# Kernel tuning notes

Measured on AMD Instinct MI355X. Metric: run time of the kernel, lower is better.

Reference implementation:

```python
import jax, jax.numpy as jnp
import numpy as np

N_NODES = 50000
N_EDGES = 800000
NEG_SLOPE = 0.2


def _gat_layer(x, src, dst, W, al, ar, n_nodes):
    """Single multi-head GAT conv (DGL-style). Returns [N, H, D]."""
    H, D = al.shape
    feat = (x @ W).reshape(n_nodes, H, D)              # [N,H,D]
    el = jnp.einsum('nhd,hd->nh', feat, al)            # [N,H]
    er = jnp.einsum('nhd,hd->nh', feat, ar)            # [N,H]
    e = jax.nn.leaky_relu(el[src] + er[dst], NEG_SLOPE)  # [E,H]
    # numerically-stable edge softmax over incoming edges per dst node
    emax = jax.ops.segment_max(e, dst, num_segments=n_nodes)  # [N,H]
    emax = jnp.where(jnp.isfinite(emax), emax, 0.0)
    ee = jnp.exp(e - emax[dst])                        # [E,H]
    denom = jax.ops.segment_sum(ee, dst, num_segments=n_nodes)  # [N,H]
    alpha = ee / (denom[dst] + 1e-9)                   # [E,H]
    msg = alpha[:, :, None] * feat[src]                # [E,H,D]
    return jax.ops.segment_sum(msg, dst, num_segments=n_nodes)  # [N,H,D]


def setup_inputs() -> dict:
    key = jax.random.key(0)
    ks = jax.random.split(key, 9)
    features = jax.random.normal(ks[0], (N_NODES, 512), jnp.float32)
    src = jax.random.randint(ks[1], (N_EDGES,), 0, N_NODES)
    dst = jax.random.randint(ks[2], (N_EDGES,), 0, N_NODES)
    W1 = jax.random.normal(ks[3], (512, 256), jnp.float32) * 0.05
    al1 = jax.random.normal(ks[4], (8, 32), jnp.float32) * 0.05
    ar1 = jax.random.normal(ks[5], (8, 32), jnp.float32) * 0.05
    W2 = jax.random.normal(ks[6], (256, 320), jnp.float32) * 0.05
    al2 = jax.random.normal(ks[7], (8, 40), jnp.float32) * 0.05
    ar2 = jax.random.normal(ks[8], (8, 40), jnp.float32) * 0.05
    return {"features": features, "src": src, "dst": dst,
            "W1": W1, "al1": al1, "ar1": ar1,
            "W2": W2, "al2": al2, "ar2": ar2}


def reference(features, src, dst, W1, al1, ar1, W2, al2, ar2):
    n = features.shape[0]
    h = _gat_layer(features, src, dst, W1, al1, ar1, n)   # [N,8,32]
    h = jax.nn.elu(h.reshape(n, -1))                      # flatten(1) + ELU -> [N,256]
    h = _gat_layer(h, src, dst, W2, al2, ar2, n)          # [N,8,40]
    return h.mean(axis=1)                                 # head mean -> [N,40]
```

## Files before the change

kernel.cpp:

```cpp
#include <hip/hip_runtime.h>
#include <math.h>

typedef float f32x4 __attribute__((ext_vector_type(4)));
typedef __bf16 bf16x2 __attribute__((ext_vector_type(2)));
typedef __bf16 bf16x4 __attribute__((ext_vector_type(4)));
typedef __bf16 bf16x8 __attribute__((ext_vector_type(8)));


__global__ void hist_kernel(const int* __restrict__ dst, int* __restrict__ cnt, int E) {
    int e = blockIdx.x * blockDim.x + threadIdx.x;
    if (e < E) atomicAdd(&cnt[dst[e]], 1);
}

__global__ __launch_bounds__(256) void scan_blk(const int* __restrict__ cnt,
                                                int* __restrict__ incl,
                                                int* __restrict__ bsum, int n) {
    __shared__ int sd[256];
    const int t = threadIdx.x;
    int i = blockIdx.x * 256 + t;
    int v = (i < n) ? cnt[i] : 0;
    sd[t] = v;
    __syncthreads();
#pragma unroll
    for (int off = 1; off < 256; off <<= 1) {
        int x = (t >= off) ? sd[t - off] : 0;
        __syncthreads();
        sd[t] += x;
        __syncthreads();
    }
    if (i < n) incl[i] = sd[t];
    if (t == 255) bsum[blockIdx.x] = sd[255];
}

__global__ __launch_bounds__(256) void scan_top(const int* __restrict__ bsum,
                                                int* __restrict__ boff, int nb) {
    __shared__ int sd[256];
    const int t = threadIdx.x;
    int v = (t < nb) ? bsum[t] : 0;
    sd[t] = v;
    __syncthreads();
#pragma unroll
    for (int off = 1; off < 256; off <<= 1) {
        int x = (t >= off) ? sd[t - off] : 0;
        __syncthreads();
        sd[t] += x;
        __syncthreads();
    }
    if (t < nb) boff[t] = sd[t] - v;
}

__global__ void scan_fix(const int* __restrict__ incl, const int* __restrict__ boff,
                         const int* __restrict__ cnt, int* __restrict__ row_ptr,
                         int* __restrict__ cursor, int n) {
    int i = blockIdx.x * blockDim.x + threadIdx.x;
    if (i >= n) return;
    int total = incl[i] + boff[i >> 8];
    row_ptr[i + 1] = total;
    cursor[i] = total - cnt[i];
    if (i == 0) row_ptr[0] = 0;
}

__global__ void fill_kernel(const int* __restrict__ src, const int* __restrict__ dst,
                            int* __restrict__ cursor, int* __restrict__ ssrc, int E) {
    int e = blockIdx.x * blockDim.x + threadIdx.x;
    if (e < E) {
        int pos = atomicAdd(&cursor[dst[e]], 1);
        ssrc[pos] = src[e];
    }
}

__global__ void pack_b_kernel(const float* __restrict__ W, __bf16* __restrict__ Bh,
                              int K, int N) {
    int idx = blockIdx.x * blockDim.x + threadIdx.x;
    if (idx >= K * N) return;
    int e = idx & 7;
    int l = (idx >> 3) & 63;
    int c = idx >> 9;
    int ng = N >> 4;
    int g = c % ng;
    int k0 = (c / ng) << 5;
    int col = g * 16 + (l & 15);
    int k = k0 + ((l >> 4) << 3) + e;
    Bh[idx] = (__bf16)W[(size_t)k * N + col];
}

__device__ __forceinline__ int swz6(int x) { return x ^ (x >> 3); }

template <int BN, int NREP, bool FP32A>
__global__ __launch_bounds__(256, 4) void gemm_fused(
    const float* __restrict__ Af, const __bf16* __restrict__ Ahg,
    const __bf16* __restrict__ Alg, const __bf16* __restrict__ Bph,
    const float* __restrict__ al, const float* __restrict__ ar,
    __bf16* __restrict__ featb, float* __restrict__ el, float* __restrict__ er,
    int M, int K) {
    constexpr int WN = NREP * 16;
    constexpr int D = BN / 8;

    struct StageT {
        __bf16 Ah[2][2][64][8];
        __bf16 Al[2][2][64][8];
    };
    union Smem {
        StageT s;
        float ctile[4][16][WN + 1];
    };
    __shared__ __align__(16) Smem u;

    const int t = threadIdx.x;
    const int lane = t & 63;
    const int wid = t >> 6;
    const int row0 = blockIdx.x * 32;
    const int colw = wid * WN;
    const int fr = lane & 15;
    const int kq = lane >> 4;
    const int sr = t >> 3;
    const int kc = (t & 7) * 4;
    const int m_s = sr >> 4;
    const int xs = (sr & 15) + 16 * (kc >> 3);
    const int e0 = kc & 7;

    float4 av;
    bf16x4 avh, avl;

    auto loadA = [&](int k0) {
        int gr = row0 + sr;
        if (gr >= M) gr = M - 1;
        if constexpr (FP32A) {
            av = *(const float4*)&Af[(size_t)gr * K + k0 + kc];
        } else {
            avh = *(const bf16x4*)&Ahg[(size_t)gr * K + k0 + kc];
            avl = *(const bf16x4*)&Alg[(size_t)gr * K + k0 + kc];
        }
    };
    auto storeA = [&](int p) {
        if constexpr (FP32A) {
            __bf16 h0 = (__bf16)av.x, h1 = (__bf16)av.y, h2 = (__bf16)av.z,
                   h3 = (__bf16)av.w;
            bf16x4 hv = {h0, h1, h2, h3};
            bf16x4 lv = {(__bf16)(av.x - (float)h0), (__bf16)(av.y - (float)h1),
                         (__bf16)(av.z - (float)h2), (__bf16)(av.w - (float)h3)};
            *(bf16x4*)&u.s.Ah[p][m_s][swz6(xs)][e0] = hv;
            *(bf16x4*)&u.s.Al[p][m_s][swz6(xs)][e0] = lv;
        } else {
            *(bf16x4*)&u.s.Ah[p][m_s][swz6(xs)][e0] = avh;
            *(bf16x4*)&u.s.Al[p][m_s][swz6(xs)][e0] = avl;
        }
    };

    f32x4 acc[2][NREP] = {};

    loadA(0);
    int p = 0;
    for (int k0 = 0; k0 < K; k0 += 32) {
        bf16x8 bh[NREP];
        const int c0 = (k0 >> 5) * (BN >> 4) + wid * NREP;
#pragma unroll
        for (int n = 0; n < NREP; ++n)
            bh[n] = *(const bf16x8*)&Bph[(size_t)(c0 + n) * 512 + lane * 8];
        storeA(p);
        if (k0 + 32 < K) loadA(k0 + 32);
        __syncthreads();
        const int sl_ = swz6(lane);
        bf16x8 ah0 = *(const bf16x8*)&u.s.Ah[p][0][sl_][0];
        bf16x8 ah1 = *(const bf16x8*)&u.s.Ah[p][1][sl_][0];
        bf16x8 al0 = *(const bf16x8*)&u.s.Al[p][0][sl_][0];
        bf16x8 al1 = *(const bf16x8*)&u.s.Al[p][1][sl_][0];
#pragma unroll
        for (int n = 0; n < NREP; ++n) {
            acc[0][n] = __builtin_amdgcn_mfma_f32_16x16x32_bf16(ah0, bh[n], acc[0][n], 0, 0, 0);
            acc[0][n] = __builtin_amdgcn_mfma_f32_16x16x32_bf16(al0, bh[n], acc[0][n], 0, 0, 0);
            acc[1][n] = __builtin_amdgcn_mfma_f32_16x16x32_bf16(ah1, bh[n], acc[1][n], 0, 0, 0);
            acc[1][n] = __builtin_amdgcn_mfma_f32_16x16x32_bf16(al1, bh[n], acc[1][n], 0, 0, 0);
        }
        p ^= 1;
    }

#pragma unroll
    for (int m = 0; m < 2; ++m) {
        int rbase = row0 + m * 16 + kq * 4;
#pragma unroll
        for (int n = 0; n < NREP; ++n) {
            int col = colw + n * 16 + fr;
#pragma unroll
            for (int i = 0; i < 4; ++i) {
                int r = rbase + i;
                if (r < M) featb[(size_t)r * BN + col] = (__bf16)acc[m][n][i];
            }
        }
    }

    __syncthreads();
#pragma unroll
    for (int m = 0; m < 2; ++m) {
#pragma unroll
        for (int n = 0; n < NREP; ++n)
#pragma unroll
            for (int i = 0; i < 4; ++i)
                u.ctile[wid][kq * 4 + i][n * 16 + fr] = acc[m][n][i];
        if (lane < 32) {
            int r = lane & 15;
            int hh = lane >> 4;
            int h = wid * 2 + hh;
            float sl = 0.f, sr_ = 0.f;
#pragma unroll 8
            for (int d = 0; d < D; ++d) {
                float v = u.ctile[wid][r][hh * D + d];
                sl += v * al[h * D + d];
                sr_ += v * ar[h * D + d];
            }
            int gr = row0 + m * 16 + r;
            if (gr < M) {
                el[(size_t)gr * 8 + h] = sl;
                er[(size_t)gr * 8 + h] = sr_;
            }
        }
    }
}

__device__ __forceinline__ float leaky02(float x) { return x > 0.f ? x : 0.2f * x; }

template <int D, int MODE>
__global__ __launch_bounds__(256) void gat_aggregate(
    const __bf16* __restrict__ featb, const float* __restrict__ el,
    const float* __restrict__ er, const int* __restrict__ row_ptr,
    const int* __restrict__ ssrc, __bf16* __restrict__ outh,
    __bf16* __restrict__ outl, float* __restrict__ outf, int N) {
    constexpr int HD = 8 * D;
    constexpr int TAIL = HD - 256;
    __shared__ float red[4][MODE ? HD : 1];

    const int wid = threadIdx.x >> 6;
    const int lane = threadIdx.x & 63;
    const int n = blockIdx.x * 4 + wid;
    if (n >= N) return;

    const int beg = row_ptr[n];
    const int end = row_ptr[n + 1];
    const int hl = lane & 7;
    const int sl = lane >> 3;
    const float er_l = er[(size_t)n * 8 + hl];

    float s_l = 0.f;
    int idx = beg + sl;
    for (; idx + 8 < end; idx += 16) {
        int s0 = ssrc[idx];
        int s1 = ssrc[idx + 8];
        float e0 = el[(size_t)s0 * 8 + hl];
        float e1 = el[(size_t)s1 * 8 + hl];
        s_l += __expf(leaky02(e0 + er_l)) + __expf(leaky02(e1 + er_l));
    }
    if (idx < end)
        s_l += __expf(leaky02(el[(size_t)ssrc[idx] * 8 + hl] + er_l));
    s_l += __shfl_xor(s_l, 8);
    s_l += __shfl_xor(s_l, 16);
    s_l += __shfl_xor(s_l, 32);
    const float si_l = 1.0f / (s_l + 1e-9f);

    int hg[2], ht = 0;
#pragma unroll
    for (int g = 0; g < 2; ++g) hg[g] = (128 * g + 2 * lane) / D;
    if (TAIL) ht = (256 + lane) / D;

    float acc[2][2] = {};
    float acct = 0.f;
    idx = beg;
    for (; idx + 4 <= end; idx += 4) {
        int ss[4];
#pragma unroll
        for (int uu = 0; uu < 4; ++uu) ss[uu] = ssrc[idx + uu];
        float aa[4];
#pragma unroll
        for (int uu = 0; uu < 4; ++uu)
            aa[uu] = __expf(leaky02(el[(size_t)ss[uu] * 8 + hl] + er_l)) * si_l;
        bf16x2 p[4][2];
        __bf16 pt[4];
#pragma unroll
        for (int uu = 0; uu < 4; ++uu) {
            const __bf16* f = featb + (size_t)ss[uu] * HD;
            p[uu][0] = *(const bf16x2*)&f[2 * lane];
            p[uu][1] = *(const bf16x2*)&f[128 + 2 * lane];
            if (TAIL) pt[uu] = f[256 + lane];
        }
#pragma unroll
        for (int uu = 0; uu < 4; ++uu) {
            float w0 = __shfl(aa[uu], hg[0]);
            float w1 = __shfl(aa[uu], hg[1]);
            acc[0][0] += w0 * (float)p[uu][0].x;
            acc[0][1] += w0 * (float)p[uu][0].y;
            acc[1][0] += w1 * (float)p[uu][1].x;
            acc[1][1] += w1 * (float)p[uu][1].y;
            if (TAIL) {
                float wt = __shfl(aa[uu], ht);
                acct += wt * (float)pt[uu];
            }
        }
    }
    for (; idx < end; ++idx) {
        int s = ssrc[idx];
        float a = __expf(leaky02(el[(size_t)s * 8 + hl] + er_l)) * si_l;
        const __bf16* f = featb + (size_t)s * HD;
        float w0 = __shfl(a, hg[0]);
        float w1 = __shfl(a, hg[1]);
        bf16x2 p0 = *(const bf16x2*)&f[2 * lane];
        bf16x2 p1 = *(const bf16x2*)&f[128 + 2 * lane];
        acc[0][0] += w0 * (float)p0.x;
        acc[0][1] += w0 * (float)p0.y;
        acc[1][0] += w1 * (float)p1.x;
        acc[1][1] += w1 * (float)p1.y;
        if (TAIL) {
            float wt = __shfl(a, ht);
            acct += wt * (float)f[256 + lane];
        }
    }

    if (MODE == 0) {
#pragma unroll
        for (int g = 0; g < 2; ++g) {
            float x0 = acc[g][0], x1 = acc[g][1];
            x0 = x0 > 0.f ? x0 : expm1f(x0);
            x1 = x1 > 0.f ? x1 : expm1f(x1);
            __bf16 h0 = (__bf16)x0, h1 = (__bf16)x1;
            bf16x2 vh = {h0, h1};
            bf16x2 vl = {(__bf16)(x0 - (float)h0), (__bf16)(x1 - (float)h1)};
            *(bf16x2*)&outh[(size_t)n * 256 + 128 * g + 2 * lane] = vh;
            *(bf16x2*)&outl[(size_t)n * 256 + 128 * g + 2 * lane] = vl;
        }
    } else {
#pragma unroll
        for (int g = 0; g < 2; ++g) {
            red[wid][128 * g + 2 * lane] = acc[g][0];
            red[wid][128 * g + 2 * lane + 1] = acc[g][1];
        }
        red[wid][256 + lane] = acct;
        if (lane < D) {
            float s = 0.f;
#pragma unroll
            for (int hh = 0; hh < 8; ++hh) s += red[wid][hh * D + lane];
            outf[(size_t)n * D + lane] = s * 0.125f;
        }
    }
}


extern "C" void kernel_launch(void* const* d_in, const int* in_sizes, int n_in,
                              void* d_out, int out_size, void* d_ws, size_t ws_size,
                              hipStream_t stream) {
    const float* features = (const float*)d_in[0];
    const int* src = (const int*)d_in[1];
    const int* dst = (const int*)d_in[2];
    const float* W1 = (const float*)d_in[3];
    const float* al1 = (const float*)d_in[4];
    const float* ar1 = (const float*)d_in[5];
    const float* W2 = (const float*)d_in[6];
    const float* al2 = (const float*)d_in[7];
    const float* ar2 = (const float*)d_in[8];

    const int N = in_sizes[0] / 512;
    const int E = in_sizes[1];

    char* ws = (char*)d_ws;
    size_t off = 0;
    auto alloc = [&](size_t bytes) -> void* {
        void* p = ws + off;
        off = (off + bytes + 255) & ~(size_t)255;
        return p;
    };
    __bf16* feat1b = (__bf16*)alloc((size_t)N * 256 * 2);
    __bf16* h_hi = (__bf16*)alloc((size_t)N * 256 * 2);
    __bf16* h_lo = (__bf16*)alloc((size_t)N * 256 * 2);
    __bf16* feat2b = (__bf16*)alloc((size_t)N * 320 * 2);
    float* el1 = (float*)alloc((size_t)N * 8 * 4);
    float* er1 = (float*)alloc((size_t)N * 8 * 4);
    float* el2 = (float*)alloc((size_t)N * 8 * 4);
    float* er2 = (float*)alloc((size_t)N * 8 * 4);
    int* cnt = (int*)alloc((size_t)N * 4);
    int* incl = (int*)alloc((size_t)N * 4);
    int* row_ptr = (int*)alloc((size_t)(N + 1) * 4);
    int* cursor = (int*)alloc((size_t)N * 4);
    int* bsum = (int*)alloc(256 * 4);
    int* boff = (int*)alloc(256 * 4);
    int* ssrc = (int*)alloc((size_t)E * 4);
    __bf16* Bp1h = (__bf16*)alloc((size_t)512 * 256 * 2);
    __bf16* Bp2h = (__bf16*)alloc((size_t)256 * 320 * 2);

    const int NB = (N + 255) / 256;

    hipMemsetAsync(cnt, 0, (size_t)N * 4, stream);
    hist_kernel<<<(E + 255) / 256, 256, 0, stream>>>(dst, cnt, E);
    scan_blk<<<NB, 256, 0, stream>>>(cnt, incl, bsum, N);
    scan_top<<<1, 256, 0, stream>>>(bsum, boff, NB);
    scan_fix<<<NB, 256, 0, stream>>>(incl, boff, cnt, row_ptr, cursor, N);
    fill_kernel<<<(E + 255) / 256, 256, 0, stream>>>(src, dst, cursor, ssrc, E);

    pack_b_kernel<<<(512 * 256 + 255) / 256, 256, 0, stream>>>(W1, Bp1h, 512, 256);
    pack_b_kernel<<<(256 * 320 + 255) / 256, 256, 0, stream>>>(W2, Bp2h, 256, 320);

    const int mblk = (N + 31) / 32;

    gemm_fused<256, 4, true><<<mblk, 256, 0, stream>>>(
        features, nullptr, nullptr, Bp1h, al1, ar1, feat1b, el1, er1, N, 512);
    gat_aggregate<32, 0><<<(N + 3) / 4, 256, 0, stream>>>(
        feat1b, el1, er1, row_ptr, ssrc, h_hi, h_lo, nullptr, N);

    gemm_fused<320, 5, false><<<mblk, 256, 0, stream>>>(
        nullptr, h_hi, h_lo, Bp2h, al2, ar2, feat2b, el2, er2, N, 256);
    gat_aggregate<40, 1><<<(N + 3) / 4, 256, 0, stream>>>(
        feat2b, el2, er2, row_ptr, ssrc, nullptr, nullptr, (float*)d_out, N);
}
```

Baseline: 329.2 us.

## Drop bf16 split for layer-2 input, prefetch B, cache edge weights in LDS

```diff
diff --git a/kernel.cpp b/kernel.cpp
--- a/kernel.cpp
+++ b/kernel.cpp
@@ -86,13 +86,12 @@
 
 __device__ __forceinline__ int swz6(int x) { return x ^ (x >> 3); }
 
-template <int BN, int NREP, bool FP32A>
+template <int BN, int NREP, bool FP32A, int TERMS>
 __global__ __launch_bounds__(256, 4) void gemm_fused(
     const float* __restrict__ Af, const __bf16* __restrict__ Ahg,
-    const __bf16* __restrict__ Alg, const __bf16* __restrict__ Bph,
-    const float* __restrict__ al, const float* __restrict__ ar,
-    __bf16* __restrict__ featb, float* __restrict__ el, float* __restrict__ er,
-    int M, int K) {
+    const __bf16* __restrict__ Bph, const float* __restrict__ al,
+    const float* __restrict__ ar, __bf16* __restrict__ featb,
+    float* __restrict__ el, float* __restrict__ er, int M, int K) {
     constexpr int WN = NREP * 16;
     constexpr int D = BN / 8;
 
@@ -120,7 +119,7 @@
     const int e0 = kc & 7;
 
     float4 av;
-    bf16x4 avh, avl;
+    bf16x4 avh;
 
     auto loadA = [&](int k0) {
         int gr = row0 + sr;
@@ -129,7 +128,6 @@
             av = *(const float4*)&Af[(size_t)gr * K + k0 + kc];
         } else {
             avh = *(const bf16x4*)&Ahg[(size_t)gr * K + k0 + kc];
-            avl = *(const bf16x4*)&Alg[(size_t)gr * K + k0 + kc];
         }
     };
     auto storeA = [&](int p) {
@@ -143,34 +141,49 @@
             *(bf16x4*)&u.s.Al[p][m_s][swz6(xs)][e0] = lv;
         } else {
             *(bf16x4*)&u.s.Ah[p][m_s][swz6(xs)][e0] = avh;
-            *(bf16x4*)&u.s.Al[p][m_s][swz6(xs)][e0] = avl;
-        }
+        }
+    };
+    auto loadB = [&](int k0, bf16x8* b) {
+        const int c0 = (k0 >> 5) * (BN >> 4) + wid * NREP;
+#pragma unroll
+        for (int n = 0; n < NREP; ++n)
+            b[n] = *(const bf16x8*)&Bph[(size_t)(c0 + n) * 512 + lane * 8];
     };
 
     f32x4 acc[2][NREP] = {};
+    bf16x8 bh[NREP], bn[NREP];
 
     loadA(0);
+    loadB(0, bh);
     int p = 0;
     for (int k0 = 0; k0 < K; k0 += 32) {
-        bf16x8 bh[NREP];
-        const int c0 = (k0 >> 5) * (BN >> 4) + wid * NREP;
-#pragma unroll
-        for (int n = 0; n < NREP; ++n)
-            bh[n] = *(const bf16x8*)&Bph[(size_t)(c0 + n) * 512 + lane * 8];
         storeA(p);
-        if (k0 + 32 < K) loadA(k0 + 32);
+        const bool nxt = (k0 + 32 < K);
+        if (nxt) {
+            loadA(k0 + 32);
+            loadB(k0 + 32, bn);
+        }
         __syncthreads();
         const int sl_ = swz6(lane);
         bf16x8 ah0 = *(const bf16x8*)&u.s.Ah[p][0][sl_][0];
         bf16x8 ah1 = *(const bf16x8*)&u.s.Ah[p][1][sl_][0];
-        bf16x8 al0 = *(const bf16x8*)&u.s.Al[p][0][sl_][0];
-        bf16x8 al1 = *(const bf16x8*)&u.s.Al[p][1][sl_][0];
+        bf16x8 al0, al1;
+        if constexpr (TERMS == 2) {
+            al0 = *(const bf16x8*)&u.s.Al[p][0][sl_][0];
+            al1 = *(const bf16x8*)&u.s.Al[p][1][sl_][0];
+        }
 #pragma unroll
         for (int n = 0; n < NREP; ++n) {
             acc[0][n] = __builtin_amdgcn_mfma_f32_16x16x32_bf16(ah0, bh[n], acc[0][n], 0, 0, 0);
-            acc[0][n] = __builtin_amdgcn_mfma_f32_16x16x32_bf16(al0, bh[n], acc[0][n], 0, 0, 0);
             acc[1][n] = __builtin_amdgcn_mfma_f32_16x16x32_bf16(ah1, bh[n], acc[1][n], 0, 0, 0);
-            acc[1][n] = __builtin_amdgcn_mfma_f32_16x16x32_bf16(al1, bh[n], acc[1][n], 0, 0, 0);
+            if constexpr (TERMS == 2) {
+                acc[0][n] = __builtin_amdgcn_mfma_f32_16x16x32_bf16(al0, bh[n], acc[0][n], 0, 0, 0);
+                acc[1][n] = __builtin_amdgcn_mfma_f32_16x16x32_bf16(al1, bh[n], acc[1][n], 0, 0, 0);
+            }
+        }
+        if (nxt) {
+#pragma unroll
+            for (int n = 0; n < NREP; ++n) bh[n] = bn[n];
         }
         p ^= 1;
     }
@@ -224,9 +237,11 @@
     const __bf16* __restrict__ featb, const float* __restrict__ el,
     const float* __restrict__ er, const int* __restrict__ row_ptr,
     const int* __restrict__ ssrc, __bf16* __restrict__ outh,
-    __bf16* __restrict__ outl, float* __restrict__ outf, int N) {
+    float* __restrict__ outf, int N) {
     constexpr int HD = 8 * D;
     constexpr int TAIL = HD - 256;
+    constexpr int CAP = 64;
+    __shared__ float alds[4][CAP][8];
     __shared__ float red[4][MODE ? HD : 1];
 
     const int wid = threadIdx.x >> 6;
@@ -241,16 +256,13 @@
     const float er_l = er[(size_t)n * 8 + hl];
 
     float s_l = 0.f;
-    int idx = beg + sl;
-    for (; idx + 8 < end; idx += 16) {
-        int s0 = ssrc[idx];
-        int s1 = ssrc[idx + 8];
-        float e0 = el[(size_t)s0 * 8 + hl];
-        float e1 = el[(size_t)s1 * 8 + hl];
-        s_l += __expf(leaky02(e0 + er_l)) + __expf(leaky02(e1 + er_l));
-    }
-    if (idx < end)
-        s_l += __expf(leaky02(el[(size_t)ssrc[idx] * 8 + hl] + er_l));
+    for (int idx = beg + sl; idx < end; idx += 8) {
+        int s = ssrc[idx];
+        float e = __expf(leaky02(el[(size_t)s * 8 + hl] + er_l));
+        s_l += e;
+        int j = idx - beg;
+        if (j < CAP) alds[wid][j][hl] = e;
+    }
     s_l += __shfl_xor(s_l, 8);
     s_l += __shfl_xor(s_l, 16);
     s_l += __shfl_xor(s_l, 32);
@@ -263,15 +275,20 @@
 
     float acc[2][2] = {};
     float acct = 0.f;
-    idx = beg;
-    for (; idx + 4 <= end; idx += 4) {
+    const int capend = (end - beg > CAP) ? beg + CAP : end;
+    int idx = beg;
+    for (; idx + 4 <= capend; idx += 4) {
+        int j = idx - beg;
         int ss[4];
 #pragma unroll
         for (int uu = 0; uu < 4; ++uu) ss[uu] = ssrc[idx + uu];
-        float aa[4];
-#pragma unroll
-        for (int uu = 0; uu < 4; ++uu)
-            aa[uu] = __expf(leaky02(el[(size_t)ss[uu] * 8 + hl] + er_l)) * si_l;
+        float w0[4], w1[4], wt[4];
+#pragma unroll
+        for (int uu = 0; uu < 4; ++uu) {
+            w0[uu] = alds[wid][j + uu][hg[0]];
+            w1[uu] = alds[wid][j + uu][hg[1]];
+            if (TAIL) wt[uu] = alds[wid][j + uu][ht];
+        }
         bf16x2 p[4][2];
         __bf16 pt[4];
 #pragma unroll
@@ -283,21 +300,30 @@
         }
 #pragma unroll
         for (int uu = 0; uu < 4; ++uu) {
-            float w0 = __shfl(aa[uu], hg[0]);
-            float w1 = __shfl(aa[uu], hg[1]);
-            acc[0][0] += w0 * (float)p[uu][0].x;
-            acc[0][1] += w0 * (float)p[uu][0].y;
-            acc[1][0] += w1 * (float)p[uu][1].x;
-            acc[1][1] += w1 * (float)p[uu][1].y;
-            if (TAIL) {
-                float wt = __shfl(aa[uu], ht);
-                acct += wt * (float)pt[uu];
-            }
-        }
+            acc[0][0] += w0[uu] * (float)p[uu][0].x;
+            acc[0][1] += w0[uu] * (float)p[uu][0].y;
+            acc[1][0] += w1[uu] * (float)p[uu][1].x;
+            acc[1][1] += w1[uu] * (float)p[uu][1].y;
+            if (TAIL) acct += wt[uu] * (float)pt[uu];
+        }
+    }
+    for (; idx < capend; ++idx) {
+        int j = idx - beg;
+        int s = ssrc[idx];
+        float w0 = alds[wid][j][hg[0]];
+        float w1 = alds[wid][j][hg[1]];
+        const __bf16* f = featb + (size_t)s * HD;
+        bf16x2 p0 = *(const bf16x2*)&f[2 * lane];
+        bf16x2 p1 = *(const bf16x2*)&f[128 + 2 * lane];
+        acc[0][0] += w0 * (float)p0.x;
+        acc[0][1] += w0 * (float)p0.y;
+        acc[1][0] += w1 * (float)p1.x;
+        acc[1][1] += w1 * (float)p1.y;
+        if (TAIL) acct += alds[wid][j][ht] * (float)f[256 + lane];
     }
     for (; idx < end; ++idx) {
         int s = ssrc[idx];
-        float a = __expf(leaky02(el[(size_t)s * 8 + hl] + er_l)) * si_l;
+        float a = __expf(leaky02(el[(size_t)s * 8 + hl] + er_l));
         const __bf16* f = featb + (size_t)s * HD;
         float w0 = __shfl(a, hg[0]);
         float w1 = __shfl(a, hg[1]);
@@ -307,11 +333,16 @@
         acc[0][1] += w0 * (float)p0.y;
         acc[1][0] += w1 * (float)p1.x;
         acc[1][1] += w1 * (float)p1.y;
-        if (TAIL) {
-            float wt = __shfl(a, ht);
-            acct += wt * (float)f[256 + lane];
-        }
-    }
+        if (TAIL) acct += __shfl(a, ht) * (float)f[256 + lane];
+    }
+
+    const float si0 = __shfl(si_l, hg[0]);
+    const float si1 = __shfl(si_l, hg[1]);
+    acc[0][0] *= si0;
+    acc[0][1] *= si0;
+    acc[1][0] *= si1;
+    acc[1][1] *= si1;
+    if (TAIL) acct *= __shfl(si_l, ht);
 
     if (MODE == 0) {
 #pragma unroll
@@ -319,11 +350,8 @@
             float x0 = acc[g][0], x1 = acc[g][1];
             x0 = x0 > 0.f ? x0 : expm1f(x0);
             x1 = x1 > 0.f ? x1 : expm1f(x1);
-            __bf16 h0 = (__bf16)x0, h1 = (__bf16)x1;
-            bf16x2 vh = {h0, h1};
-            bf16x2 vl = {(__bf16)(x0 - (float)h0), (__bf16)(x1 - (float)h1)};
+            bf16x2 vh = {(__bf16)x0, (__bf16)x1};
             *(bf16x2*)&outh[(size_t)n * 256 + 128 * g + 2 * lane] = vh;
-            *(bf16x2*)&outl[(size_t)n * 256 + 128 * g + 2 * lane] = vl;
         }
     } else {
 #pragma unroll
@@ -366,8 +394,7 @@
         return p;
     };
     __bf16* feat1b = (__bf16*)alloc((size_t)N * 256 * 2);
-    __bf16* h_hi = (__bf16*)alloc((size_t)N * 256 * 2);
-    __bf16* h_lo = (__bf16*)alloc((size_t)N * 256 * 2);
+    __bf16* hbuf = (__bf16*)alloc((size_t)N * 256 * 2);
     __bf16* feat2b = (__bf16*)alloc((size_t)N * 320 * 2);
     float* el1 = (float*)alloc((size_t)N * 8 * 4);
     float* er1 = (float*)alloc((size_t)N * 8 * 4);
@@ -397,13 +424,13 @@
 
     const int mblk = (N + 31) / 32;
 
-    gemm_fused<256, 4, true><<<mblk, 256, 0, stream>>>(
-        features, nullptr, nullptr, Bp1h, al1, ar1, feat1b, el1, er1, N, 512);
+    gemm_fused<256, 4, true, 2><<<mblk, 256, 0, stream>>>(
+        features, nullptr, Bp1h, al1, ar1, feat1b, el1, er1, N, 512);
     gat_aggregate<32, 0><<<(N + 3) / 4, 256, 0, stream>>>(
-        feat1b, el1, er1, row_ptr, ssrc, h_hi, h_lo, nullptr, N);
-
-    gemm_fused<320, 5, false><<<mblk, 256, 0, stream>>>(
-        nullptr, h_hi, h_lo, Bp2h, al2, ar2, feat2b, el2, er2, N, 256);
+        feat1b, el1, er1, row_ptr, ssrc, hbuf, nullptr, N);
+
+    gemm_fused<320, 5, false, 1><<<mblk, 256, 0, stream>>>(
+        nullptr, hbuf, Bp2h, al2, ar2, feat2b, el2, er2, N, 256);
     gat_aggregate<40, 1><<<(N + 3) / 4, 256, 0, stream>>>(
-        feat2b, el2, er2, row_ptr, ssrc, nullptr, nullptr, (float*)d_out, N);
-}
+        feat2b, el2, er2, row_ptr, ssrc, nullptr, (float*)d_out, N);
+}
```

New measurement: 320.1 us. 1.03x faster.
